# Performance work log

Measured on AMD Instinct MI355X. Metric: run time of the kernel, lower is better.

The kernel has to match this reference:

```python
import jax, jax.numpy as jnp
import numpy as np

DIM = 1024
N_HEADS = 16
HEAD_DIM = DIM // N_HEADS  # 64
FF_DIM = 4096
BATCH = 2
SEQ = 2048
EPS = 1e-8
ROPE_BASE = 10000.0


def _rope_cos_sin(seq_len, head_dim):
    # inv_freq: [head_dim//2]
    inv_freq = 1.0 / (ROPE_BASE ** (jnp.arange(0, head_dim, 2, dtype=jnp.float32) / head_dim))
    t = jnp.arange(seq_len, dtype=jnp.float32)
    freqs = jnp.einsum('i,j->ij', t, inv_freq)          # [S, D/2]
    emb = jnp.concatenate([freqs, freqs], axis=-1)       # [S, D]
    return jnp.cos(emb), jnp.sin(emb)


def _apply_rope(x, cos, sin):
    # x: [B, S, H, D]; cos/sin: [S, D] -> broadcast [1, S, 1, D]
    d2 = x.shape[-1] // 2
    x1, x2 = x[..., :d2], x[..., d2:]
    cos = cos[None, :, None, :]
    sin = sin[None, :, None, :]
    cos1, cos2 = cos[..., :d2], cos[..., d2:]
    sin1, sin2 = sin[..., :d2], sin[..., d2:]
    return jnp.concatenate([x1 * cos1 - x2 * sin1, x1 * sin2 + x2 * cos2], axis=-1)


def _rmsnorm(x, scale):
    # norm = ||x||_2 * d^{-1/2}; out = scale * x / (norm + eps)
    norm = jnp.sqrt(jnp.sum(x * x, axis=-1, keepdims=True)) * (x.shape[-1] ** -0.5)
    return scale * x / (norm + EPS)


def setup_inputs() -> dict:
    key = jax.random.key(0)
    ks = jax.random.split(key, 10)
    s = lambda fan_in: 1.0 / np.sqrt(fan_in)
    return {
        'x': jax.random.normal(ks[0], (BATCH, SEQ, DIM), dtype=jnp.float32),
        'w_qkv': jax.random.normal(ks[1], (DIM, 3 * DIM), dtype=jnp.float32) * s(DIM),
        'w_attn_out': jax.random.normal(ks[2], (DIM, DIM), dtype=jnp.float32) * s(DIM),
        'w_gate': jax.random.normal(ks[3], (DIM, FF_DIM), dtype=jnp.float32) * s(DIM),
        'b_gate': jax.random.normal(ks[4], (FF_DIM,), dtype=jnp.float32) * 0.01,
        'w_lin': jax.random.normal(ks[5], (DIM, FF_DIM), dtype=jnp.float32) * s(DIM),
        'b_lin': jax.random.normal(ks[6], (FF_DIM,), dtype=jnp.float32) * 0.01,
        'w_ff_out': jax.random.normal(ks[7], (FF_DIM, DIM), dtype=jnp.float32) * s(FF_DIM),
        'scale1': jnp.ones((DIM,), dtype=jnp.float32),
        'scale2': jnp.ones((DIM,), dtype=jnp.float32),
    }


def reference(x, w_qkv, w_attn_out, w_gate, b_gate, w_lin, b_lin, w_ff_out, scale1, scale2):
    B, S, _ = x.shape
    residual = x
    qkv = (x @ w_qkv).reshape(B, S, 3, N_HEADS, HEAD_DIM)
    q, k, v = qkv[:, :, 0], qkv[:, :, 1], qkv[:, :, 2]  # [B, S, H, D]
    cos, sin = _rope_cos_sin(S, HEAD_DIM)
    q = _apply_rope(q, cos, sin)
    k = _apply_rope(k, cos, sin)
    # attention scores [B, H, S, S]
    attn = jnp.einsum('bqhd,bkhd->bhqk', q, k) / np.sqrt(HEAD_DIM).astype(np.float32)
    attn = jax.nn.softmax(attn, axis=-1)
    out = jnp.einsum('bhqk,bkhd->bqhd', attn, v).reshape(B, S, DIM)
    out = out @ w_attn_out
    x = _rmsnorm(residual + out, scale1)
    residual = x
    ff = jax.nn.sigmoid(x @ w_gate + b_gate) * (x @ w_lin + b_lin)
    ff = ff @ w_ff_out
    x = _rmsnorm(residual + ff, scale2)
    return x
```

## Files before the change

### kernel.cpp

```cpp
#include <hip/hip_runtime.h>
#include <stdint.h>

#define DIMN 1024
#define NH 16
#define HD 64
#define FFN 4096
#define BBATCH 2
#define SSEQ 2048
#define MROWS (BBATCH*SSEQ)

typedef __bf16 bf16;
typedef __bf16 bf16x8 __attribute__((ext_vector_type(8)));
typedef __bf16 bf16x4 __attribute__((ext_vector_type(4)));
typedef float f32x4 __attribute__((ext_vector_type(4)));
typedef float f32x16 __attribute__((ext_vector_type(16)));
typedef uint32_t u32x4 __attribute__((ext_vector_type(4)));

#define AS1 __attribute__((address_space(1)))
#define AS3 __attribute__((address_space(3)))

__device__ __forceinline__ void gload16(const bf16* g, bf16* l) {
  __builtin_amdgcn_global_load_lds((AS1 const void*)g, (AS3 void*)l, 16, 0, 0);
}

__device__ __forceinline__ uint32_t pkbf(float a, float b) {
  union { bf16 h[2]; uint32_t u; } x;
  x.h[0] = (bf16)a; x.h[1] = (bf16)b;
  return x.u;
}

__global__ void rope_table_kernel(float* __restrict__ tab) {
  int i = blockIdx.x * blockDim.x + threadIdx.x;
  int s = i >> 5, d = i & 31;
  float invf = exp2f(-(float)d * 0.4152410118609203f);
  float fr = (float)s * invf;
  tab[s*64 + d]      = cosf(fr);
  tab[s*64 + 32 + d] = sinf(fr);
}

__global__ void cast_f32_bf16(const float* __restrict__ in, bf16* __restrict__ out, int n4) {
  int i = blockIdx.x * blockDim.x + threadIdx.x;
  if (i < n4) {
    f32x4 v = ((const f32x4*)in)[i];
    bf16x4 o = {(bf16)v.x, (bf16)v.y, (bf16)v.z, (bf16)v.w};
    ((bf16x4*)out)[i] = o;
  }
}

__global__ __launch_bounds__(256) void transpose_cast_f32_bf16(
    const float* __restrict__ in, bf16* __restrict__ out, int R, int C) {
  __shared__ float t[32][33];
  int bx = blockIdx.x, by = blockIdx.y;
  int x = threadIdx.x, y = threadIdx.y;
  #pragma unroll
  for (int j = 0; j < 4; ++j) {
    int r = by*32 + y*4 + j;
    t[y*4+j][x] = in[(size_t)r*C + bx*32 + x];
  }
  __syncthreads();
  #pragma unroll
  for (int j = 0; j < 4; ++j) {
    int c = bx*32 + y*4 + j;
    out[(size_t)c*R + by*32 + x] = (bf16)t[x][y*4+j];
  }
}

__global__ __launch_bounds__(256) void pack_wfrag(
    const float* __restrict__ W, bf16* __restrict__ WF, int K, int N) {
  int g = blockIdx.x * 4 + (threadIdx.x >> 6);
  int l = threadIdx.x & 63;
  int KT = K >> 5;
  int n  = g & 3;
  int kt = (g >> 2) % KT;
  int cb = (g >> 2) / KT;
  int c  = cb*64 + n*16 + (l & 15);
  int k0 = kt*32 + (l >> 4)*8;
  bf16x8 v;
  #pragma unroll
  for (int j = 0; j < 8; ++j) v[j] = (bf16)W[(size_t)(k0 + j)*N + c];
  *(bf16x8*)&WF[((size_t)g*64 + l)*8] = v;
}

template<int NP>
__global__ __launch_bounds__(256) void rmsnorm_sum_kernel(
    const float* __restrict__ parts, const float* __restrict__ resid,
    const float* __restrict__ sc,
    float* __restrict__ outf, bf16* __restrict__ outb) {
  int row = blockIdx.x;
  int tid = threadIdx.x;
  size_t off = (size_t)row * DIMN;
  f32x4 v = ((const f32x4*)(resid + off))[tid];
  #pragma unroll
  for (int p = 0; p < NP; ++p) {
    f32x4 a = ((const f32x4*)(parts + (size_t)p * MROWS * DIMN + off))[tid];
    v.x += a.x; v.y += a.y; v.z += a.z; v.w += a.w;
  }
  float ss = v.x*v.x + v.y*v.y + v.z*v.z + v.w*v.w;
  #pragma unroll
  for (int m = 1; m < 64; m <<= 1) ss += __shfl_xor(ss, m);
  __shared__ float red[4];
  if ((tid & 63) == 0) red[tid >> 6] = ss;
  __syncthreads();
  float tot = red[0] + red[1] + red[2] + red[3];
  float inv = 1.f / (sqrtf(tot) * 0.03125f + 1e-8f);
  f32x4 s4 = ((const f32x4*)sc)[tid];
  f32x4 o = {v.x*s4.x*inv, v.y*s4.y*inv, v.z*s4.z*inv, v.w*s4.w*inv};
  if (outf) ((f32x4*)(outf + off))[tid] = o;
  if (outb) {
    bf16x4 ob = {(bf16)o.x, (bf16)o.y, (bf16)o.z, (bf16)o.w};
    ((bf16x4*)(outb + off))[tid] = ob;
  }
}

template<int EPI>
__global__ void __launch_bounds__(256, 2) gemm_bt(
    const bf16* __restrict__ A, const bf16* __restrict__ B,
    int M, int N, int K,
    void* __restrict__ o0, void* __restrict__ o1, void* __restrict__ o2,
    const void* __restrict__ a0, const void* __restrict__ a1) {
  __shared__ __align__(16) bf16 sh_a[2*4096];
  __shared__ __align__(16) bf16 sh_b[2*4096];
  const int tid  = threadIdx.x;
  const int lane = tid & 63;
  const int wid  = tid >> 6;

  int gx  = gridDim.x;
  int bid = blockIdx.y * gx + blockIdx.x;
  int nwg = gx * gridDim.y;
  int cpx = nwg >> 3;
  int swz = (bid & 7) * cpx + (bid >> 3);
  int bxi = swz % gx, byi = swz / gx;

  const int m0 = byi * 128, n0 = bxi * 128;
  const int wm = (wid >> 1) * 64, wn = (wid & 1) * 64;

  const int kb = blockIdx.z;
  const int KC = K / (int)gridDim.z;

  f32x4 acc[4][4] = {};

  const bf16* a_base = A + (size_t)m0 * K + (size_t)kb * KC;
  const bf16* b_base = B + (size_t)n0 * K + (size_t)kb * KC;

  auto stage = [&](int kt, int buf) {
    const int lb = buf * 4096;
    #pragma unroll
    for (int i = 0; i < 2; ++i) {
      int idx = i*256 + tid;
      size_t go = (size_t)(idx >> 2)*K + (size_t)kt*32 + (idx & 3)*8;
      gload16(a_base + go, &sh_a[lb + idx*8]);
    }
    #pragma unroll
    for (int i = 0; i < 2; ++i) {
      int idx = i*256 + tid;
      size_t go = (size_t)(idx >> 2)*K + (size_t)kt*32 + (idx & 3)*8;
      gload16(b_base + go, &sh_b[lb + idx*8]);
    }
  };

  const int nsteps = KC >> 5;
  stage(0, 0);
  for (int t = 0; t < nsteps; ++t) {
    const int cb = t & 1;
    if (t + 1 < nsteps) {
      stage(t+1, cb ^ 1);
      asm volatile("s_waitcnt vmcnt(4)" ::: "memory");
    } else {
      asm volatile("s_waitcnt vmcnt(0)" ::: "memory");
    }
    __builtin_amdgcn_sched_barrier(0);
    __builtin_amdgcn_s_barrier();
    __builtin_amdgcn_sched_barrier(0);

    const int lb = cb * 4096;
    bf16x8 af[4], bfr[4];
    #pragma unroll
    for (int m = 0; m < 4; ++m)
      af[m] = *(const bf16x8*)&sh_a[lb + (wm + m*16 + (lane & 15))*32 + (lane >> 4)*8];
    #pragma unroll
    for (int n = 0; n < 4; ++n)
      bfr[n] = *(const bf16x8*)&sh_b[lb + (wn + n*16 + (lane & 15))*32 + (lane >> 4)*8];
    __builtin_amdgcn_s_setprio(1);
    #pragma unroll
    for (int m = 0; m < 4; ++m)
      #pragma unroll
      for (int n = 0; n < 4; ++n)
        acc[m][n] = __builtin_amdgcn_mfma_f32_16x16x32_bf16(af[m], bfr[n], acc[m][n], 0, 0, 0);
    __builtin_amdgcn_s_setprio(0);
    __builtin_amdgcn_sched_barrier(0);
    __builtin_amdgcn_s_barrier();
  }

  const int rq = (lane >> 4) * 4;
  const int cl = lane & 15;

  if constexpr (EPI == 0) {
    bf16* q_p = (bf16*)o0; bf16* k_p = (bf16*)o1; bf16* v_p = (bf16*)o2;
    const float* rope = (const float*)a0;
    int sec = (n0 + wn) >> 10;
    int h   = ((n0 + wn) & 1023) >> 6;
    const float qsc = (sec == 0) ? 0.18033688011112042f : 1.0f;
    #pragma unroll
    for (int m = 0; m < 4; ++m) {
      #pragma unroll
      for (int reg = 0; reg < 4; ++reg) {
        int r  = m0 + wm + m*16 + rq + reg;
        int b_ = r >> 11, s_ = r & 2047;
        int tile = s_ >> 5;
        size_t tb = ((size_t)(b_*NH + h) * 64 + tile) * 2048;
        if (sec == 2) {
          int kvl = s_ & 31;
          int ks = kvl >> 4, hiv = (kvl >> 3) & 1, jv = kvl & 7;
          #pragma unroll
          for (int n = 0; n < 4; ++n) {
            int half = n >> 1;
            int qlv  = (n & 1) * 16 + cl;
            v_p[tb + (size_t)(ks*2 + half)*512 + (hiv*32 + qlv)*8 + jv] =
                (bf16)acc[m][n][reg];
          }
        } else {
          int qlt = s_ & 31;
          bf16* dst = (sec == 0 ? q_p : k_p);
          int lo = ((cl >> 3) * 32 + qlt) * 8 + (cl & 7);
          #pragma unroll
          for (int n = 0; n < 2; ++n) {
            int d1 = n*16 + cl;
            float c1 = rope[s_*64 + d1];
            float s1 = rope[s_*64 + 32 + d1];
            float x1 = acc[m][n][reg], x2 = acc[m][n+2][reg];
            dst[tb + (size_t)n*512 + lo]       = (bf16)((x1*c1 - x2*s1) * qsc);
            dst[tb + (size_t)(n+2)*512 + lo]   = (bf16)((x1*s1 + x2*c1) * qsc);
          }
        }
      }
    }
  } else if constexpr (EPI == 4) {
    float* op = (float*)o0 + (size_t)kb * M * N;
    #pragma unroll
    for (int m = 0; m < 4; ++m)
      #pragma unroll
      for (int n = 0; n < 4; ++n)
        #pragma unroll
        for (int reg = 0; reg < 4; ++reg) {
          int r = m0 + wm + m*16 + rq + reg;
          int c = n0 + wn + n*16 + cl;
          op[(size_t)r*N + c] = acc[m][n][reg];
        }
  }
}

__global__ void __launch_bounds__(256, 2) gemm_ffn1_rw(
    const bf16* __restrict__ A, const bf16* __restrict__ WgF,
    const bf16* __restrict__ WlF, int M, int N, int K,
    bf16* __restrict__ o0, const float* __restrict__ bgv,
    const float* __restrict__ blv) {
  __shared__ __align__(16) bf16 sh_a[2*4096];
  const int tid  = threadIdx.x;
  const int lane = tid & 63;
  const int wid  = tid >> 6;

  int gx  = gridDim.x;
  int bid = blockIdx.y * gx + blockIdx.x;
  int nwg = gx * gridDim.y;
  int cpx = nwg >> 3;
  int swz = (bid & 7) * cpx + (bid >> 3);
  int bxi = swz % gx, byi = swz / gx;

  const int m0 = byi * 128, n0 = bxi * 128;
  const int wm = (wid >> 1) * 64, wn = (wid & 1) * 64;

  const int KT = K >> 5;
  const int wcb = (n0 + wn) >> 6;
  const bf16* wg = WgF + (size_t)wcb * KT * 2048;
  const bf16* wl = WlF + (size_t)wcb * KT * 2048;
  const bf16* a_base = A + (size_t)m0 * K;

  auto stageA = [&](int kt, int buf) {
    #pragma unroll
    for (int i = 0; i < 2; ++i) {
      int idx = i*256 + tid;
      size_t go = (size_t)(idx >> 2)*K + (size_t)kt*32 + (idx & 3)*8;
      gload16(a_base + go, &sh_a[buf*4096 + idx*8]);
    }
  };
  auto ldW = [&](int kt, bf16x8* bb, bf16x8* cc) {
    #pragma unroll
    for (int n = 0; n < 4; ++n) {
      bb[n] = *(const bf16x8*)&wg[(size_t)kt*2048 + n*512 + lane*8];
      cc[n] = *(const bf16x8*)&wl[(size_t)kt*2048 + n*512 + lane*8];
    }
  };

  f32x4 acc[4][4] = {}, acc2[4][4] = {};
  bf16x8 bcur[4], ccur[4], bnxt[4], cnxt[4];

  ldW(0, bcur, ccur);
  stageA(0, 0);
  for (int t = 0; t < KT; ++t) {
    const int cb = t & 1;
    if (t + 1 < KT) {
      ldW(t+1, bnxt, cnxt);
      stageA(t+1, cb ^ 1);
      asm volatile("s_waitcnt vmcnt(10)" ::: "memory");
    } else {
      asm volatile("s_waitcnt vmcnt(0)" ::: "memory");
    }
    __builtin_amdgcn_sched_barrier(0);
    __builtin_amdgcn_s_barrier();
    __builtin_amdgcn_sched_barrier(0);

    const int lb = cb * 4096;
    bf16x8 af[4];
    #pragma unroll
    for (int m = 0; m < 4; ++m)
      af[m] = *(const bf16x8*)&sh_a[lb + (wm + m*16 + (lane & 15))*32 + (lane >> 4)*8];
    __builtin_amdgcn_s_setprio(1);
    #pragma unroll
    for (int m = 0; m < 4; ++m)
      #pragma unroll
      for (int n = 0; n < 4; ++n) {
        acc [m][n] = __builtin_amdgcn_mfma_f32_16x16x32_bf16(af[m], bcur[n], acc [m][n], 0, 0, 0);
        acc2[m][n] = __builtin_amdgcn_mfma_f32_16x16x32_bf16(af[m], ccur[n], acc2[m][n], 0, 0, 0);
      }
    __builtin_amdgcn_s_setprio(0);
    __builtin_amdgcn_sched_barrier(0);
    __builtin_amdgcn_s_barrier();
    if (t + 1 < KT) {
      #pragma unroll
      for (int n = 0; n < 4; ++n) { bcur[n] = bnxt[n]; ccur[n] = cnxt[n]; }
    }
  }

  const int rq = (lane >> 4) * 4;
  const int cl = lane & 15;
  #pragma unroll
  for (int m = 0; m < 4; ++m)
    #pragma unroll
    for (int n = 0; n < 4; ++n)
      #pragma unroll
      for (int reg = 0; reg < 4; ++reg) {
        int r = m0 + wm + m*16 + rq + reg;
        int c = n0 + wn + n*16 + cl;
        float gv = acc [m][n][reg] + bgv[c];
        float lv = acc2[m][n][reg] + blv[c];
        float sg = 1.f / (1.f + __expf(-gv));
        o0[(size_t)r*N + c] = (bf16)(sg * lv);
      }
}

__global__ void __launch_bounds__(256) attn_kernel(
    const bf16* __restrict__ qf_g, const bf16* __restrict__ kf_g,
    const bf16* __restrict__ vf_g, bf16* __restrict__ ao_g) {
  __shared__ __align__(16) bf16 lds_k[2*2048];
  __shared__ __align__(16) bf16 lds_v[2*2048];
  const int tid  = threadIdx.x;
  const int lane = tid & 63;
  const int qw   = tid >> 6;
  const int hi   = lane >> 5;
  const int ql   = lane & 31;
  const int bh   = blockIdx.y;
  const int b_   = bh >> 4, h = bh & 15;
  const int q0   = blockIdx.x * 128 + qw * 32;
  const int qt   = blockIdx.x * 4 + qw;

  const bf16* qtile = qf_g + ((size_t)bh*64 + qt) * 2048;
  const bf16* kbase = kf_g + (size_t)bh * 64 * 2048;
  const bf16* vbase = vf_g + (size_t)bh * 64 * 2048;

  bf16x8 qf[4];
  #pragma unroll
  for (int ds = 0; ds < 4; ++ds)
    qf[ds] = *(const bf16x8*)&qtile[ds*512 + lane*8];

  f32x16 o0 = {}, o1 = {};
  float lrun = 0.f;

  gload16(kbase + tid*8, &lds_k[tid*8]);
  gload16(vbase + tid*8, &lds_v[tid*8]);

  for (int t = 0; t < 64; ++t) {
    const int cur = (t & 1) * 2048;
    if (t < 63) {
      const int nxt = 2048 - cur;
      gload16(kbase + (size_t)(t+1)*2048 + tid*8, &lds_k[nxt + tid*8]);
      gload16(vbase + (size_t)(t+1)*2048 + tid*8, &lds_v[nxt + tid*8]);
      asm volatile("s_waitcnt vmcnt(2)" ::: "memory");
    } else {
      asm volatile("s_waitcnt vmcnt(0)" ::: "memory");
    }
    __builtin_amdgcn_sched_barrier(0);
    __builtin_amdgcn_s_barrier();
    __builtin_amdgcn_sched_barrier(0);

    f32x16 st = {};
    __builtin_amdgcn_s_setprio(1);
    #pragma unroll
    for (int ds = 0; ds < 4; ++ds) {
      bf16x8 kf = *(const bf16x8*)&lds_k[cur + ds*512 + lane*8];
      st = __builtin_amdgcn_mfma_f32_32x32x16_bf16(kf, qf[ds], st, 0, 0, 0);
    }
    __builtin_amdgcn_s_setprio(0);
    float p[16];
    float psum = 0.f;
    #pragma unroll
    for (int r = 0; r < 16; ++r) { p[r] = __builtin_amdgcn_exp2f(st[r]); psum += p[r]; }
    lrun += psum;

    uint32_t w0 = pkbf(p[0],p[1]),   w1 = pkbf(p[2],p[3]);
    uint32_t w2 = pkbf(p[4],p[5]),   w3 = pkbf(p[6],p[7]);
    uint32_t w4 = pkbf(p[8],p[9]),   w5 = pkbf(p[10],p[11]);
    uint32_t w6 = pkbf(p[12],p[13]), w7 = pkbf(p[14],p[15]);
    asm("v_permlane32_swap_b32 %0, %1" : "+v"(w0), "+v"(w2));
    asm("v_permlane32_swap_b32 %0, %1" : "+v"(w1), "+v"(w3));
    asm("v_permlane32_swap_b32 %0, %1" : "+v"(w4), "+v"(w6));
    asm("v_permlane32_swap_b32 %0, %1" : "+v"(w5), "+v"(w7));

    __builtin_amdgcn_s_setprio(1);
    {
      union { u32x4 u; bf16x8 b; } pu;
      u32x4 pwa = {w0, w1, w2, w3};
      pu.u = pwa;
      bf16x8 v0 = *(const bf16x8*)&lds_v[cur + 0*512 + lane*8];
      bf16x8 v1 = *(const bf16x8*)&lds_v[cur + 1*512 + lane*8];
      o0 = __builtin_amdgcn_mfma_f32_32x32x16_bf16(v0, pu.b, o0, 0, 0, 0);
      o1 = __builtin_amdgcn_mfma_f32_32x32x16_bf16(v1, pu.b, o1, 0, 0, 0);
      u32x4 pwb = {w4, w5, w6, w7};
      pu.u = pwb;
      bf16x8 v2 = *(const bf16x8*)&lds_v[cur + 2*512 + lane*8];
      bf16x8 v3 = *(const bf16x8*)&lds_v[cur + 3*512 + lane*8];
      o0 = __builtin_amdgcn_mfma_f32_32x32x16_bf16(v2, pu.b, o0, 0, 0, 0);
      o1 = __builtin_amdgcn_mfma_f32_32x32x16_bf16(v3, pu.b, o1, 0, 0, 0);
    }
    __builtin_amdgcn_s_setprio(0);

    __builtin_amdgcn_sched_barrier(0);
    __builtin_amdgcn_s_barrier();
    __builtin_amdgcn_sched_barrier(0);
  }

  lrun += __shfl_xor(lrun, 32);
  float inv = 1.f / lrun;
  bf16* aop = ao_g + ((size_t)(b_*SSEQ) + q0 + ql) * DIMN + h*HD;
  #pragma unroll
  for (int g = 0; g < 4; ++g) {
    int dbase = 8*g + 4*hi;
    bf16x4 w0 = {(bf16)(o0[4*g]*inv), (bf16)(o0[4*g+1]*inv),
                 (bf16)(o0[4*g+2]*inv), (bf16)(o0[4*g+3]*inv)};
    *(bf16x4*)&aop[dbase] = w0;
    bf16x4 w1 = {(bf16)(o1[4*g]*inv), (bf16)(o1[4*g+1]*inv),
                 (bf16)(o1[4*g+2]*inv), (bf16)(o1[4*g+3]*inv)};
    *(bf16x4*)&aop[32 + dbase] = w1;
  }
}

extern "C" void kernel_launch(void* const* d_in, const int* in_sizes, int n_in,
                              void* d_out, int out_size, void* d_ws, size_t ws_size,
                              hipStream_t stream) {
  const float* x      = (const float*)d_in[0];
  const float* w_qkv  = (const float*)d_in[1];
  const float* w_ao   = (const float*)d_in[2];
  const float* w_gate = (const float*)d_in[3];
  const float* b_gate = (const float*)d_in[4];
  const float* w_lin  = (const float*)d_in[5];
  const float* b_lin  = (const float*)d_in[6];
  const float* w_ffo  = (const float*)d_in[7];
  const float* scale1 = (const float*)d_in[8];
  const float* scale2 = (const float*)d_in[9];
  float* out = (float*)d_out;
  (void)ws_size; (void)in_sizes; (void)n_in; (void)out_size;

  uint8_t* ws = (uint8_t*)d_ws;
  bf16*  wt_ws   = (bf16*) (ws + 0);
  float* rope_ws = (float*)(ws + 8388608);
  bf16*  xb_ws   = (bf16*) (ws + 8912896);
  bf16*  ao_ws   = (bf16*) (ws + 8912896);
  bf16*  q_ws    = (bf16*) (ws + 17301504);
  bf16*  k_ws    = (bf16*) (ws + 25690112);
  bf16*  v_ws    = (bf16*) (ws + 34078720);
  float* p1_ws   = (float*)(ws + 17301504);
  bf16*  wt2_ws  = (bf16*) (ws + 50855936);
  bf16*  h1b_ws  = (bf16*) (ws + 84410368);
  bf16*  ffb_ws  = (bf16*) (ws + 8912896);
  float* p2_ws   = (float*)(ws + 42467328);
  float* h1f_ws  = (float*)(ws + 109576192);

  rope_table_kernel<<<256, 256, 0, stream>>>(rope_ws);
  cast_f32_bf16<<<4096, 256, 0, stream>>>(x, xb_ws, MROWS*DIMN/4);
  transpose_cast_f32_bf16<<<dim3(3*DIMN/32, DIMN/32), dim3(32,8), 0, stream>>>(w_qkv, wt_ws, DIMN, 3*DIMN);
  gemm_bt<0><<<dim3(24, 32), 256, 0, stream>>>(xb_ws, wt_ws, MROWS, 3*DIMN, DIMN,
                                               q_ws, k_ws, v_ws, rope_ws, nullptr);
  attn_kernel<<<dim3(16, 32), 256, 0, stream>>>(q_ws, k_ws, v_ws, ao_ws);
  transpose_cast_f32_bf16<<<dim3(DIMN/32, DIMN/32), dim3(32,8), 0, stream>>>(w_ao, wt_ws, DIMN, DIMN);
  gemm_bt<4><<<dim3(8, 32, 2), 256, 0, stream>>>(ao_ws, wt_ws, MROWS, DIMN, DIMN,
                                                 p1_ws, nullptr, nullptr, nullptr, nullptr);
  rmsnorm_sum_kernel<2><<<MROWS, 256, 0, stream>>>(p1_ws, x, scale1, h1f_ws, h1b_ws);
  pack_wfrag<<<2048, 256, 0, stream>>>(w_gate, wt_ws, DIMN, FFN);
  pack_wfrag<<<2048, 256, 0, stream>>>(w_lin, wt2_ws, DIMN, FFN);
  gemm_ffn1_rw<<<dim3(32, 32), 256, 0, stream>>>(h1b_ws, wt_ws, wt2_ws, MROWS, FFN, DIMN,
                                                 ffb_ws, b_gate, b_lin);
  transpose_cast_f32_bf16<<<dim3(DIMN/32, FFN/32), dim3(32,8), 0, stream>>>(w_ffo, wt_ws, FFN, DIMN);
  gemm_bt<4><<<dim3(8, 32, 4), 256, 0, stream>>>(ffb_ws, wt_ws, MROWS, DIMN, FFN,
                                                 p2_ws, nullptr, nullptr, nullptr, nullptr);
  rmsnorm_sum_kernel<4><<<MROWS, 256, 0, stream>>>(p2_ws, h1f_ws, scale2, out, nullptr);
}
```

Measured before the change: 308.7 us.

## Load pre-packed weight fragments directly into registers in remaining GEMMs

Replaces the transpose-cast weight prep and LDS-staged B operand in the QKV, attention-out and FFN-out GEMMs with the fragment-packed layout already used by the FFN1 kernel. Each wave loads its B fragments straight from global memory into registers, double-buffered in registers. This halves LDS use so occupancy is raised to 3 blocks per SM. The cost is more global traffic for B, since the two waves sharing the same columns each load them separately, and higher register pressure from the extra fragment buffer.

```diff
diff --git a/kernel.cpp b/kernel.cpp
--- a/kernel.cpp
+++ b/kernel.cpp
@@ -44,24 +44,6 @@
     f32x4 v = ((const f32x4*)in)[i];
     bf16x4 o = {(bf16)v.x, (bf16)v.y, (bf16)v.z, (bf16)v.w};
     ((bf16x4*)out)[i] = o;
-  }
-}
-
-__global__ __launch_bounds__(256) void transpose_cast_f32_bf16(
-    const float* __restrict__ in, bf16* __restrict__ out, int R, int C) {
-  __shared__ float t[32][33];
-  int bx = blockIdx.x, by = blockIdx.y;
-  int x = threadIdx.x, y = threadIdx.y;
-  #pragma unroll
-  for (int j = 0; j < 4; ++j) {
-    int r = by*32 + y*4 + j;
-    t[y*4+j][x] = in[(size_t)r*C + bx*32 + x];
-  }
-  __syncthreads();
-  #pragma unroll
-  for (int j = 0; j < 4; ++j) {
-    int c = bx*32 + y*4 + j;
-    out[(size_t)c*R + by*32 + x] = (bf16)t[x][y*4+j];
   }
 }
 
@@ -113,13 +95,12 @@
 }
 
 template<int EPI>
-__global__ void __launch_bounds__(256, 2) gemm_bt(
-    const bf16* __restrict__ A, const bf16* __restrict__ B,
+__global__ void __launch_bounds__(256, 3) gemm_rw(
+    const bf16* __restrict__ A, const bf16* __restrict__ WF,
     int M, int N, int K,
     void* __restrict__ o0, void* __restrict__ o1, void* __restrict__ o2,
-    const void* __restrict__ a0, const void* __restrict__ a1) {
+    const void* __restrict__ a0) {
   __shared__ __align__(16) bf16 sh_a[2*4096];
-  __shared__ __align__(16) bf16 sh_b[2*4096];
   const int tid  = threadIdx.x;
   const int lane = tid & 63;
   const int wid  = tid >> 6;
@@ -136,35 +117,38 @@
 
   const int kb = blockIdx.z;
   const int KC = K / (int)gridDim.z;
-
-  f32x4 acc[4][4] = {};
-
+  const int KT = K >> 5;
+  const int nt = KC >> 5;
+
+  const int wcb = (n0 + wn) >> 6;
+  const bf16* wf = WF + (size_t)wcb * KT * 2048;
   const bf16* a_base = A + (size_t)m0 * K + (size_t)kb * KC;
-  const bf16* b_base = B + (size_t)n0 * K + (size_t)kb * KC;
-
-  auto stage = [&](int kt, int buf) {
-    const int lb = buf * 4096;
+
+  auto stageA = [&](int kt, int buf) {
     #pragma unroll
     for (int i = 0; i < 2; ++i) {
       int idx = i*256 + tid;
       size_t go = (size_t)(idx >> 2)*K + (size_t)kt*32 + (idx & 3)*8;
-      gload16(a_base + go, &sh_a[lb + idx*8]);
-    }
-    #pragma unroll
-    for (int i = 0; i < 2; ++i) {
-      int idx = i*256 + tid;
-      size_t go = (size_t)(idx >> 2)*K + (size_t)kt*32 + (idx & 3)*8;
-      gload16(b_base + go, &sh_b[lb + idx*8]);
+      gload16(a_base + go, &sh_a[buf*4096 + idx*8]);
     }
   };
-
-  const int nsteps = KC >> 5;
-  stage(0, 0);
-  for (int t = 0; t < nsteps; ++t) {
+  auto ldW = [&](int kta, bf16x8* bb) {
+    #pragma unroll
+    for (int n = 0; n < 4; ++n)
+      bb[n] = *(const bf16x8*)&wf[(size_t)kta*2048 + n*512 + lane*8];
+  };
+
+  f32x4 acc[4][4] = {};
+  bf16x8 bcur[4], bnxt[4];
+
+  ldW(kb*nt, bcur);
+  stageA(0, 0);
+  for (int t = 0; t < nt; ++t) {
     const int cb = t & 1;
-    if (t + 1 < nsteps) {
-      stage(t+1, cb ^ 1);
-      asm volatile("s_waitcnt vmcnt(4)" ::: "memory");
+    if (t + 1 < nt) {
+      ldW(kb*nt + t + 1, bnxt);
+      stageA(t+1, cb ^ 1);
+      asm volatile("s_waitcnt vmcnt(6)" ::: "memory");
     } else {
       asm volatile("s_waitcnt vmcnt(0)" ::: "memory");
     }
@@ -173,22 +157,23 @@
     __builtin_amdgcn_sched_barrier(0);
 
     const int lb = cb * 4096;
-    bf16x8 af[4], bfr[4];
+    bf16x8 af[4];
     #pragma unroll
     for (int m = 0; m < 4; ++m)
       af[m] = *(const bf16x8*)&sh_a[lb + (wm + m*16 + (lane & 15))*32 + (lane >> 4)*8];
-    #pragma unroll
-    for (int n = 0; n < 4; ++n)
-      bfr[n] = *(const bf16x8*)&sh_b[lb + (wn + n*16 + (lane & 15))*32 + (lane >> 4)*8];
     __builtin_amdgcn_s_setprio(1);
     #pragma unroll
     for (int m = 0; m < 4; ++m)
       #pragma unroll
       for (int n = 0; n < 4; ++n)
-        acc[m][n] = __builtin_amdgcn_mfma_f32_16x16x32_bf16(af[m], bfr[n], acc[m][n], 0, 0, 0);
+        acc[m][n] = __builtin_amdgcn_mfma_f32_16x16x32_bf16(af[m], bcur[n], acc[m][n], 0, 0, 0);
     __builtin_amdgcn_s_setprio(0);
     __builtin_amdgcn_sched_barrier(0);
     __builtin_amdgcn_s_barrier();
+    if (t + 1 < nt) {
+      #pragma unroll
+      for (int n = 0; n < 4; ++n) bcur[n] = bnxt[n];
+    }
   }
 
   const int rq = (lane >> 4) * 4;
@@ -486,20 +471,20 @@
 
   rope_table_kernel<<<256, 256, 0, stream>>>(rope_ws);
   cast_f32_bf16<<<4096, 256, 0, stream>>>(x, xb_ws, MROWS*DIMN/4);
-  transpose_cast_f32_bf16<<<dim3(3*DIMN/32, DIMN/32), dim3(32,8), 0, stream>>>(w_qkv, wt_ws, DIMN, 3*DIMN);
-  gemm_bt<0><<<dim3(24, 32), 256, 0, stream>>>(xb_ws, wt_ws, MROWS, 3*DIMN, DIMN,
-                                               q_ws, k_ws, v_ws, rope_ws, nullptr);
+  pack_wfrag<<<1536, 256, 0, stream>>>(w_qkv, wt_ws, DIMN, 3*DIMN);
+  gemm_rw<0><<<dim3(24, 32), 256, 0, stream>>>(xb_ws, wt_ws, MROWS, 3*DIMN, DIMN,
+                                               q_ws, k_ws, v_ws, rope_ws);
   attn_kernel<<<dim3(16, 32), 256, 0, stream>>>(q_ws, k_ws, v_ws, ao_ws);
-  transpose_cast_f32_bf16<<<dim3(DIMN/32, DIMN/32), dim3(32,8), 0, stream>>>(w_ao, wt_ws, DIMN, DIMN);
-  gemm_bt<4><<<dim3(8, 32, 2), 256, 0, stream>>>(ao_ws, wt_ws, MROWS, DIMN, DIMN,
-                                                 p1_ws, nullptr, nullptr, nullptr, nullptr);
+  pack_wfrag<<<512, 256, 0, stream>>>(w_ao, wt_ws, DIMN, DIMN);
+  gemm_rw<4><<<dim3(8, 32, 2), 256, 0, stream>>>(ao_ws, wt_ws, MROWS, DIMN, DIMN,
+                                                 p1_ws, nullptr, nullptr, nullptr);
   rmsnorm_sum_kernel<2><<<MROWS, 256, 0, stream>>>(p1_ws, x, scale1, h1f_ws, h1b_ws);
   pack_wfrag<<<2048, 256, 0, stream>>>(w_gate, wt_ws, DIMN, FFN);
   pack_wfrag<<<2048, 256, 0, stream>>>(w_lin, wt2_ws, DIMN, FFN);
   gemm_ffn1_rw<<<dim3(32, 32), 256, 0, stream>>>(h1b_ws, wt_ws, wt2_ws, MROWS, FFN, DIMN,
                                                  ffb_ws, b_gate, b_lin);
-  transpose_cast_f32_bf16<<<dim3(DIMN/32, FFN/32), dim3(32,8), 0, stream>>>(w_ffo, wt_ws, FFN, DIMN);
-  gemm_bt<4><<<dim3(8, 32, 4), 256, 0, stream>>>(ffb_ws, wt_ws, MROWS, DIMN, FFN,
-                                                 p2_ws, nullptr, nullptr, nullptr, nullptr);
+  pack_wfrag<<<2048, 256, 0, stream>>>(w_ffo, wt_ws, FFN, DIMN);
+  gemm_rw<4><<<dim3(8, 32, 4), 256, 0, stream>>>(ffb_ws, wt_ws, MROWS, DIMN, FFN,
+                                                 p2_ws, nullptr, nullptr, nullptr);
   rmsnorm_sum_kernel<4><<<MROWS, 256, 0, stream>>>(p2_ws, h1f_ws, scale2, out, nullptr);
 }
```

Result: no change. 304.3 us (-1.4%).
